# Performance work log

Measured on AMD Instinct MI355X. Metric: run time of the kernel, lower is better.

## Reference

```python
import jax, jax.numpy as jnp
import numpy as np
from jax import lax

H = 64            # hidden size
NUM_LAYERS = 3
EMBED_LEN = 128
B, T = 256, 2048


def _lstm_layer(x, Wih, Whh, bih, bhh):
    """x: [B, T, in]; returns full hidden sequence [B, T, H].
    PyTorch gate order: i, f, g, o."""
    Bn = x.shape[0]
    b = bih + bhh  # [4H]
    # Precompute input contribution for all timesteps: [T, B, 4H]
    xg = jnp.einsum('bti,gi->tbg', x, Wih) + b
    h0 = jnp.zeros((Bn, H), x.dtype)
    c0 = jnp.zeros((Bn, H), x.dtype)

    def step(carry, xg_t):
        h, c = carry
        gates = xg_t + h @ Whh.T  # [B, 4H]
        i, f, g, o = jnp.split(gates, 4, axis=-1)
        i = jax.nn.sigmoid(i)
        f = jax.nn.sigmoid(f)
        g = jnp.tanh(g)
        o = jax.nn.sigmoid(o)
        c = f * c + i * g
        h = o * jnp.tanh(c)
        return (h, c), h

    (_, _), hs = lax.scan(step, (h0, c0), xg)  # hs: [T, B, H]
    return jnp.swapaxes(hs, 0, 1)              # [B, T, H]


def setup_inputs() -> dict:
    key = jax.random.key(0)
    ks = jax.random.split(key, 20)
    k = 1.0 / np.sqrt(H)  # PyTorch default init bound

    def u(kk, shape):
        return jax.random.uniform(kk, shape, jnp.float32, -k, k)

    inp = {"x": jax.random.normal(ks[0], (B, 1, T), jnp.float32)}
    in_sizes = [1, H, H]
    idx = 1
    for l in range(NUM_LAYERS):
        inp[f"Wih{l}"] = u(ks[idx], (4 * H, in_sizes[l])); idx += 1
        inp[f"Whh{l}"] = u(ks[idx], (4 * H, H)); idx += 1
        inp[f"bih{l}"] = u(ks[idx], (4 * H,)); idx += 1
        inp[f"bhh{l}"] = u(ks[idx], (4 * H,)); idx += 1
    inp["fcW"] = u(ks[idx], (EMBED_LEN, H)); idx += 1
    inp["fcb"] = u(ks[idx], (EMBED_LEN,))
    return inp


def reference(x, Wih0, Whh0, bih0, bhh0,
              Wih1, Whh1, bih1, bhh1,
              Wih2, Whh2, bih2, bhh2,
              fcW, fcb):
    # forward: transpose [B,1,T] -> [B,T,1]
    h = jnp.swapaxes(x, 1, 2)
    h = _lstm_layer(h, Wih0, Whh0, bih0, bhh0)
    h = _lstm_layer(h, Wih1, Whh1, bih1, bhh1)
    h = _lstm_layer(h, Wih2, Whh2, bih2, bhh2)
    last = h[:, -1, :]              # [B, H]
    return last @ fcW.T + fcb       # [B, EMBED_LEN]
```

## Files before the change

### kernel.cpp

```cpp
#include <hip/hip_runtime.h>

#define T_LEN 2048
#define HID 64
#define EMB 128
#define WD 8
#define NWIN (T_LEN / WD)
#define NPH (NWIN + 4)

typedef _Float16 half2_t __attribute__((ext_vector_type(2)));
typedef unsigned uint4v __attribute__((ext_vector_type(4)));

#if __has_builtin(__builtin_amdgcn_exp2f)
#define EXP2F(x) __builtin_amdgcn_exp2f(x)
#else
#define EXP2F(x) exp2f(x)
#endif
#if __has_builtin(__builtin_amdgcn_rcpf)
#define RCPF(x) __builtin_amdgcn_rcpf(x)
#else
#define RCPF(x) (1.0f / (x))
#endif

#define LOG2E 1.4426950408889634f

__device__ __forceinline__ float fdot2(unsigned a, unsigned b, float c) {
    return __builtin_amdgcn_fdot2(__builtin_bit_cast(half2_t, a),
                                  __builtin_bit_cast(half2_t, b), c, false);
}

__device__ __forceinline__ float dotrow(const uint4v* w, const uint4v* g, float init) {
    float a0 = init, a1 = 0.f, a2 = 0.f, a3 = 0.f;
    #pragma unroll
    for (int q = 0; q < 8; ++q) {
        a0 = fdot2(w[q][0], g[q][0], a0);
        a1 = fdot2(w[q][1], g[q][1], a1);
        a2 = fdot2(w[q][2], g[q][2], a2);
        a3 = fdot2(w[q][3], g[q][3], a3);
    }
    return (a0 + a1) + (a2 + a3);
}

__device__ __forceinline__ float dot64_i8s(const uint4v* wq, const int* hs,
                                           float fs, float ext) {
    int a0 = 0, a1 = 0, a2 = 0, a3 = 0;
    #pragma unroll
    for (int q = 0; q < 4; ++q) {
        a0 = __builtin_amdgcn_sdot4((int)wq[q][0], hs[4 * q + 0], a0, false);
        a1 = __builtin_amdgcn_sdot4((int)wq[q][1], hs[4 * q + 1], a1, false);
        a2 = __builtin_amdgcn_sdot4((int)wq[q][2], hs[4 * q + 2], a2, false);
        a3 = __builtin_amdgcn_sdot4((int)wq[q][3], hs[4 * q + 3], a3, false);
    }
    int s = (a0 + a1) + (a2 + a3);
    return fmaf((float)s, fs, ext);
}

__device__ __forceinline__ void pack_h(float hf, int lane, int* hs) {
    int qv = (((int)rintf(hf * 127.f)) & 0xff) << (8 * (lane & 3));
    qv |= __builtin_amdgcn_update_dpp(0, qv, 0xB1, 0xf, 0xf, false);
    qv |= __builtin_amdgcn_update_dpp(0, qv, 0x4E, 0xf, 0xf, false);
    #pragma unroll
    for (int k = 0; k < 16; ++k) hs[k] = __builtin_amdgcn_readlane(qv, 4 * k);
}

__device__ __forceinline__ unsigned pack4i8(float4 v, float s) {
    int q0 = (int)rintf(v.x * s), q1 = (int)rintf(v.y * s);
    int q2 = (int)rintf(v.z * s), q3 = (int)rintf(v.w * s);
    return (unsigned)((q0 & 0xff) | ((q1 & 0xff) << 8) |
                      ((q2 & 0xff) << 16) | ((q3 & 0xff) << 24));
}

__device__ __forceinline__ float quant_row(const float* __restrict__ Wp, uint4v* dst) {
    const float4* p = reinterpret_cast<const float4*>(Wp);
    float m = 1e-8f;
    #pragma unroll
    for (int k = 0; k < 16; ++k) {
        float4 v = p[k];
        m = fmaxf(m, fmaxf(fmaxf(fabsf(v.x), fabsf(v.y)),
                           fmaxf(fabsf(v.z), fabsf(v.w))));
    }
    const float s = 127.f / m;
    #pragma unroll
    for (int k = 0; k < 4; ++k) {
        uint4v q;
        q[0] = pack4i8(p[4 * k + 0], s);
        q[1] = pack4i8(p[4 * k + 1], s);
        q[2] = pack4i8(p[4 * k + 2], s);
        q[3] = pack4i8(p[4 * k + 3], s);
        dst[k] = q;
    }
    return m;
}

__device__ __forceinline__ uint4v pack8(float4 a, float4 b, float s) {
    half2_t h0{(_Float16)(a.x * s), (_Float16)(a.y * s)};
    half2_t h1{(_Float16)(a.z * s), (_Float16)(a.w * s)};
    half2_t h2{(_Float16)(b.x * s), (_Float16)(b.y * s)};
    half2_t h3{(_Float16)(b.z * s), (_Float16)(b.w * s)};
    uint4v q;
    q[0] = __builtin_bit_cast(unsigned, h0);
    q[1] = __builtin_bit_cast(unsigned, h1);
    q[2] = __builtin_bit_cast(unsigned, h2);
    q[3] = __builtin_bit_cast(unsigned, h3);
    return q;
}

__device__ __forceinline__ void cvt8(const float* __restrict__ Wp, float s, uint4v* dst) {
    const float4* p = reinterpret_cast<const float4*>(Wp);
    #pragma unroll
    for (int k = 0; k < 8; ++k) dst[k] = pack8(p[2 * k], p[2 * k + 1], s);
}

__global__ __launch_bounds__(512)
__attribute__((amdgpu_waves_per_eu(2, 2)))
void lstm3_fused(
    const float* __restrict__ x,
    const float* __restrict__ Wih0, const float* __restrict__ Whh0,
    const float* __restrict__ bih0, const float* __restrict__ bhh0,
    const float* __restrict__ Wih1, const float* __restrict__ Whh1,
    const float* __restrict__ bih1, const float* __restrict__ bhh1,
    const float* __restrict__ Wih2, const float* __restrict__ Whh2,
    const float* __restrict__ bih2, const float* __restrict__ bhh2,
    const float* __restrict__ fcW,  const float* __restrict__ fcb,
    float* __restrict__ out)
{
    const int b   = blockIdx.x;
    const int tid = threadIdx.x;
    const int wv  = tid >> 6;
    const int L   = tid & 63;

    __shared__ __align__(16) _Float16 h0ring[16][HID];
    __shared__ __align__(16) _Float16 h1ring[16][HID];
    __shared__ __align__(16) _Float16 h2ring[2][HID];
    __shared__ float p1buf[2][WD][4][HID];
    __shared__ float p2buf[2][WD][4][HID];
    __shared__ __align__(16) float xs[T_LEN];

    {
        const float4* xg4 = reinterpret_cast<const float4*>(x + b * T_LEN);
        reinterpret_cast<float4*>(xs)[tid] = xg4[tid];
        reinterpret_cast<unsigned*>(h0ring)[tid] = 0u;
        reinterpret_cast<unsigned*>(h1ring)[tid] = 0u;
        if (tid < 64) reinterpret_cast<unsigned*>(h2ring)[tid] = 0u;
    }

    const float sI = -LOG2E, sF = -LOG2E, sG = -2.f * LOG2E, sO = -LOG2E;
    const float scl[4] = {sI, sF, sG, sO};

    uint4v w[4][8];
    uint4v wq[4][4];
    float bias4[4] = {0.f, 0.f, 0.f, 0.f};
    float wx4[4]   = {0.f, 0.f, 0.f, 0.f};
    float fs4[4]   = {0.f, 0.f, 0.f, 0.f};

    if (wv < 3) {
        const float* Wh = (wv == 0) ? Whh0 : (wv == 1) ? Whh1 : Whh2;
        const float* bi = (wv == 0) ? bih0 : (wv == 1) ? bih1 : bih2;
        const float* bh = (wv == 0) ? bhh0 : (wv == 1) ? bhh1 : bhh2;
        #pragma unroll
        for (int c = 0; c < 4; ++c) {
            float m = quant_row(Wh + (c * 64 + L) * 64, wq[c]);
            fs4[c] = scl[c] * m * (1.f / (127.f * 127.f));
            bias4[c] = (bi[c * 64 + L] + bh[c * 64 + L]) * scl[c];
        }
        if (wv == 0) {
            #pragma unroll
            for (int c = 0; c < 4; ++c) wx4[c] = Wih0[c * 64 + L] * scl[c];
        }
    } else if (wv == 4) {
        cvt8(Wih1 + (  0 + L) * 64, sI, w[0]);
    } else if (wv == 5) {
        cvt8(Wih1 + ( 64 + L) * 64, sF, w[0]);
    } else if (wv == 6) {
        cvt8(Wih1 + (128 + L) * 64, sG, w[0]);
    } else if (wv == 3) {
        cvt8(Wih1 + (192 + L) * 64, sO, w[0]);
        cvt8(Wih2 + (  0 + L) * 64, sI, w[1]);
    } else {
        cvt8(Wih2 + ( 64 + L) * 64, sF, w[0]);
        cvt8(Wih2 + (128 + L) * 64, sG, w[1]);
        cvt8(Wih2 + (192 + L) * 64, sO, w[2]);
    }

    float cst = 0.f;
    int hs[16];
    #pragma unroll
    for (int k = 0; k < 16; ++k) hs[k] = 0;

    __syncthreads();

    for (int ph = 0; ph < NPH; ++ph) {
        const int par = ph & 1;

        if (wv == 0) {
            if (ph < NWIN) {
                const int tb = ph * WD;
                #pragma unroll
                for (int j = 0; j < WD; ++j) {
                    const int r = par * 8 + j;
                    float xv = xs[tb + j];
                    float d0 = dot64_i8s(wq[0], hs, fs4[0], fmaf(wx4[0], xv, bias4[0]));
                    float d1 = dot64_i8s(wq[1], hs, fs4[1], fmaf(wx4[1], xv, bias4[1]));
                    float d2 = dot64_i8s(wq[2], hs, fs4[2], fmaf(wx4[2], xv, bias4[2]));
                    float d3 = dot64_i8s(wq[3], hs, fs4[3], fmaf(wx4[3], xv, bias4[3]));
                    float ai = RCPF(1.f + EXP2F(d0));
                    float af = RCPF(1.f + EXP2F(d1));
                    float ag = fmaf(2.f, RCPF(1.f + EXP2F(d2)), -1.f);
                    float ao = RCPF(1.f + EXP2F(d3));
                    cst = fmaf(af, cst, ai * ag);
                    float tc = fmaf(2.f, RCPF(1.f + EXP2F(-2.f * LOG2E * cst)), -1.f);
                    float hf = ao * tc;
                    h0ring[r][L] = (_Float16)hf;
                    pack_h(hf, L, hs);
                }
            }
        } else if (wv == 1) {
            if (ph >= 2 && ph < NWIN + 2) {
                const float (*pb)[4][HID] = p1buf[par];
                #pragma unroll
                for (int j = 0; j < WD; ++j) {
                    const int r = par * 8 + j;
                    float d0 = dot64_i8s(wq[0], hs, fs4[0], bias4[0] + pb[j][0][L]);
                    float d1 = dot64_i8s(wq[1], hs, fs4[1], bias4[1] + pb[j][1][L]);
                    float d2 = dot64_i8s(wq[2], hs, fs4[2], bias4[2] + pb[j][2][L]);
                    float d3 = dot64_i8s(wq[3], hs, fs4[3], bias4[3] + pb[j][3][L]);
                    float ai = RCPF(1.f + EXP2F(d0));
                    float af = RCPF(1.f + EXP2F(d1));
                    float ag = fmaf(2.f, RCPF(1.f + EXP2F(d2)), -1.f);
                    float ao = RCPF(1.f + EXP2F(d3));
                    cst = fmaf(af, cst, ai * ag);
                    float tc = fmaf(2.f, RCPF(1.f + EXP2F(-2.f * LOG2E * cst)), -1.f);
                    float hf = ao * tc;
                    h1ring[r][L] = (_Float16)hf;
                    pack_h(hf, L, hs);
                }
            }
        } else if (wv == 2) {
            if (ph >= 4) {
                const float (*pb)[4][HID] = p2buf[par];
                #pragma unroll
                for (int j = 0; j < WD; ++j) {
                    float d0 = dot64_i8s(wq[0], hs, fs4[0], bias4[0] + pb[j][0][L]);
                    float d1 = dot64_i8s(wq[1], hs, fs4[1], bias4[1] + pb[j][1][L]);
                    float d2 = dot64_i8s(wq[2], hs, fs4[2], bias4[2] + pb[j][2][L]);
                    float d3 = dot64_i8s(wq[3], hs, fs4[3], bias4[3] + pb[j][3][L]);
                    float ai = RCPF(1.f + EXP2F(d0));
                    float af = RCPF(1.f + EXP2F(d1));
                    float ag = fmaf(2.f, RCPF(1.f + EXP2F(d2)), -1.f);
                    float ao = RCPF(1.f + EXP2F(d3));
                    cst = fmaf(af, cst, ai * ag);
                    float tc = fmaf(2.f, RCPF(1.f + EXP2F(-2.f * LOG2E * cst)), -1.f);
                    float hf = ao * tc;
                    h2ring[j & 1][L] = (_Float16)hf;
                    pack_h(hf, L, hs);
                }
            }
        } else {
            const bool p1act = (ph >= 1 && ph < NWIN + 1);
            const bool p2act = (ph >= 3 && ph < NWIN + 3);
            if (wv == 4 || wv == 5 || wv == 6) {
                if (p1act) {
                    const _Float16* hw = &h0ring[(par ^ 1) * 8][0];
                    float (*po)[4][HID] = p1buf[par ^ 1];
                    const int c0 = wv - 4;
                    #pragma unroll
                    for (int j = 0; j < WD; ++j) {
                        const uint4v* hp = reinterpret_cast<const uint4v*>(hw + j * HID);
                        uint4v g[8];
                        #pragma unroll
                        for (int k = 0; k < 8; ++k) g[k] = hp[k];
                        po[j][c0][L] = dotrow(w[0], g, 0.f);
                    }
                }
            } else if (wv == 3) {
                if (p1act) {
                    const _Float16* hw = &h0ring[(par ^ 1) * 8][0];
                    float (*po)[4][HID] = p1buf[par ^ 1];
                    #pragma unroll
                    for (int j = 0; j < WD; ++j) {
                        const uint4v* hp = reinterpret_cast<const uint4v*>(hw + j * HID);
                        uint4v g[8];
                        #pragma unroll
                        for (int k = 0; k < 8; ++k) g[k] = hp[k];
                        po[j][3][L] = dotrow(w[0], g, 0.f);
                    }
                }
                if (p2act) {
                    const _Float16* hw = &h1ring[(par ^ 1) * 8][0];
                    float (*po)[4][HID] = p2buf[par ^ 1];
                    #pragma unroll
                    for (int j = 0; j < WD; ++j) {
                        const uint4v* hp = reinterpret_cast<const uint4v*>(hw + j * HID);
                        uint4v g[8];
                        #pragma unroll
                        for (int k = 0; k < 8; ++k) g[k] = hp[k];
                        po[j][0][L] = dotrow(w[1], g, 0.f);
                    }
                }
            } else {
                if (p2act) {
                    const _Float16* hw = &h1ring[(par ^ 1) * 8][0];
                    float (*po)[4][HID] = p2buf[par ^ 1];
                    #pragma unroll
                    for (int j = 0; j < WD; ++j) {
                        const uint4v* hp = reinterpret_cast<const uint4v*>(hw + j * HID);
                        uint4v g[8];
                        #pragma unroll
                        for (int k = 0; k < 8; ++k) g[k] = hp[k];
                        po[j][1][L] = dotrow(w[0], g, 0.f);
                        po[j][2][L] = dotrow(w[1], g, 0.f);
                        po[j][3][L] = dotrow(w[2], g, 0.f);
                    }
                }
            }
        }

        __syncthreads();
    }

    if (tid < EMB) {
        float acc = fcb[tid];
        const _Float16* hf = &h2ring[1][0];
        const float4* W4 = reinterpret_cast<const float4*>(fcW + tid * HID);
        #pragma unroll
        for (int k = 0; k < 16; ++k) {
            float4 wv4 = W4[k];
            acc = fmaf(wv4.x, (float)hf[4 * k + 0], acc);
            acc = fmaf(wv4.y, (float)hf[4 * k + 1], acc);
            acc = fmaf(wv4.z, (float)hf[4 * k + 2], acc);
            acc = fmaf(wv4.w, (float)hf[4 * k + 3], acc);
        }
        out[b * EMB + tid] = acc;
    }
}

extern "C" void kernel_launch(void* const* d_in, const int* in_sizes, int n_in,
                              void* d_out, int out_size, void* d_ws, size_t ws_size,
                              hipStream_t stream) {
    const float* x    = (const float*)d_in[0];
    const float* Wih0 = (const float*)d_in[1];
    const float* Whh0 = (const float*)d_in[2];
    const float* bih0 = (const float*)d_in[3];
    const float* bhh0 = (const float*)d_in[4];
    const float* Wih1 = (const float*)d_in[5];
    const float* Whh1 = (const float*)d_in[6];
    const float* bih1 = (const float*)d_in[7];
    const float* bhh1 = (const float*)d_in[8];
    const float* Wih2 = (const float*)d_in[9];
    const float* Whh2 = (const float*)d_in[10];
    const float* bih2 = (const float*)d_in[11];
    const float* bhh2 = (const float*)d_in[12];
    const float* fcW  = (const float*)d_in[13];
    const float* fcb  = (const float*)d_in[14];
    float* out = (float*)d_out;

    lstm3_fused<<<dim3(256), dim3(512), 0, stream>>>(
        x, Wih0, Whh0, bih0, bhh0,
        Wih1, Whh1, bih1, bhh1,
        Wih2, Whh2, bih2, bhh2,
        fcW, fcb, out);
}
```

Measured before the change: 948.4 us.

## Quantize input-projection weights and hidden rings to int8, consolidate onto two waves

The input projections for layers 1 and 2 switch from fp16 dot2 products on five helper waves to int8 sdot4 products. Each projection is now handled by a single wave (wave 3 for layer 1, wave 7 for layer 2), and waves 4-6 go idle. The hidden-state rings in shared memory now store int8 values instead of fp16, which halves shared reads and lets the recurrent waves reuse their existing quantized value. The trade-off is precision: the input-side weights and hidden states lose accuracy from int8 quantization. Also, each remaining helper wave does four rows per step, so it may become the critical path of each phase.

Result: faster. 878.6 us (-7.4%).

```diff
diff --git a/kernel.cpp b/kernel.cpp
--- a/kernel.cpp
+++ b/kernel.cpp
@@ -23,23 +23,6 @@
 
 #define LOG2E 1.4426950408889634f
 
-__device__ __forceinline__ float fdot2(unsigned a, unsigned b, float c) {
-    return __builtin_amdgcn_fdot2(__builtin_bit_cast(half2_t, a),
-                                  __builtin_bit_cast(half2_t, b), c, false);
-}
-
-__device__ __forceinline__ float dotrow(const uint4v* w, const uint4v* g, float init) {
-    float a0 = init, a1 = 0.f, a2 = 0.f, a3 = 0.f;
-    #pragma unroll
-    for (int q = 0; q < 8; ++q) {
-        a0 = fdot2(w[q][0], g[q][0], a0);
-        a1 = fdot2(w[q][1], g[q][1], a1);
-        a2 = fdot2(w[q][2], g[q][2], a2);
-        a3 = fdot2(w[q][3], g[q][3], a3);
-    }
-    return (a0 + a1) + (a2 + a3);
-}
-
 __device__ __forceinline__ float dot64_i8s(const uint4v* wq, const int* hs,
                                            float fs, float ext) {
     int a0 = 0, a1 = 0, a2 = 0, a3 = 0;
@@ -54,8 +37,22 @@
     return fmaf((float)s, fs, ext);
 }
 
-__device__ __forceinline__ void pack_h(float hf, int lane, int* hs) {
-    int qv = (((int)rintf(hf * 127.f)) & 0xff) << (8 * (lane & 3));
+__device__ __forceinline__ float dot64_i8v(const uint4v* wq, const uint4v* g,
+                                           float fs) {
+    int a0 = 0, a1 = 0, a2 = 0, a3 = 0;
+    #pragma unroll
+    for (int q = 0; q < 4; ++q) {
+        a0 = __builtin_amdgcn_sdot4((int)wq[q][0], (int)g[q][0], a0, false);
+        a1 = __builtin_amdgcn_sdot4((int)wq[q][1], (int)g[q][1], a1, false);
+        a2 = __builtin_amdgcn_sdot4((int)wq[q][2], (int)g[q][2], a2, false);
+        a3 = __builtin_amdgcn_sdot4((int)wq[q][3], (int)g[q][3], a3, false);
+    }
+    int s = (a0 + a1) + (a2 + a3);
+    return (float)s * fs;
+}
+
+__device__ __forceinline__ void pack_hq(int qb, int lane, int* hs) {
+    int qv = (qb & 0xff) << (8 * (lane & 3));
     qv |= __builtin_amdgcn_update_dpp(0, qv, 0xB1, 0xf, 0xf, false);
     qv |= __builtin_amdgcn_update_dpp(0, qv, 0x4E, 0xf, 0xf, false);
     #pragma unroll
@@ -89,25 +86,6 @@
         dst[k] = q;
     }
     return m;
-}
-
-__device__ __forceinline__ uint4v pack8(float4 a, float4 b, float s) {
-    half2_t h0{(_Float16)(a.x * s), (_Float16)(a.y * s)};
-    half2_t h1{(_Float16)(a.z * s), (_Float16)(a.w * s)};
-    half2_t h2{(_Float16)(b.x * s), (_Float16)(b.y * s)};
-    half2_t h3{(_Float16)(b.z * s), (_Float16)(b.w * s)};
-    uint4v q;
-    q[0] = __builtin_bit_cast(unsigned, h0);
-    q[1] = __builtin_bit_cast(unsigned, h1);
-    q[2] = __builtin_bit_cast(unsigned, h2);
-    q[3] = __builtin_bit_cast(unsigned, h3);
-    return q;
-}
-
-__device__ __forceinline__ void cvt8(const float* __restrict__ Wp, float s, uint4v* dst) {
-    const float4* p = reinterpret_cast<const float4*>(Wp);
-    #pragma unroll
-    for (int k = 0; k < 8; ++k) dst[k] = pack8(p[2 * k], p[2 * k + 1], s);
 }
 
 __global__ __launch_bounds__(512)
@@ -128,8 +106,8 @@
     const int wv  = tid >> 6;
     const int L   = tid & 63;
 
-    __shared__ __align__(16) _Float16 h0ring[16][HID];
-    __shared__ __align__(16) _Float16 h1ring[16][HID];
+    __shared__ __align__(16) signed char h0q[16][HID];
+    __shared__ __align__(16) signed char h1q[16][HID];
     __shared__ __align__(16) _Float16 h2ring[2][HID];
     __shared__ float p1buf[2][WD][4][HID];
     __shared__ float p2buf[2][WD][4][HID];
@@ -138,15 +116,16 @@
     {
         const float4* xg4 = reinterpret_cast<const float4*>(x + b * T_LEN);
         reinterpret_cast<float4*>(xs)[tid] = xg4[tid];
-        reinterpret_cast<unsigned*>(h0ring)[tid] = 0u;
-        reinterpret_cast<unsigned*>(h1ring)[tid] = 0u;
+        if (tid < 256) {
+            reinterpret_cast<unsigned*>(h0q)[tid] = 0u;
+            reinterpret_cast<unsigned*>(h1q)[tid] = 0u;
+        }
         if (tid < 64) reinterpret_cast<unsigned*>(h2ring)[tid] = 0u;
     }
 
     const float sI = -LOG2E, sF = -LOG2E, sG = -2.f * LOG2E, sO = -LOG2E;
     const float scl[4] = {sI, sF, sG, sO};
 
-    uint4v w[4][8];
     uint4v wq[4][4];
     float bias4[4] = {0.f, 0.f, 0.f, 0.f};
     float wx4[4]   = {0.f, 0.f, 0.f, 0.f};
@@ -166,19 +145,13 @@
             #pragma unroll
             for (int c = 0; c < 4; ++c) wx4[c] = Wih0[c * 64 + L] * scl[c];
         }
-    } else if (wv == 4) {
-        cvt8(Wih1 + (  0 + L) * 64, sI, w[0]);
-    } else if (wv == 5) {
-        cvt8(Wih1 + ( 64 + L) * 64, sF, w[0]);
-    } else if (wv == 6) {
-        cvt8(Wih1 + (128 + L) * 64, sG, w[0]);
-    } else if (wv == 3) {
-        cvt8(Wih1 + (192 + L) * 64, sO, w[0]);
-        cvt8(Wih2 + (  0 + L) * 64, sI, w[1]);
-    } else {
-        cvt8(Wih2 + ( 64 + L) * 64, sF, w[0]);
-        cvt8(Wih2 + (128 + L) * 64, sG, w[1]);
-        cvt8(Wih2 + (192 + L) * 64, sO, w[2]);
+    } else if (wv == 3 || wv == 7) {
+        const float* Wsrc = (wv == 3) ? Wih1 : Wih2;
+        #pragma unroll
+        for (int c = 0; c < 4; ++c) {
+            float m = quant_row(Wsrc + (c * 64 + L) * 64, wq[c]);
+            fs4[c] = scl[c] * m * (1.f / (127.f * 127.f));
+        }
     }
 
     float cst = 0.f;
@@ -209,8 +182,9 @@
                     cst = fmaf(af, cst, ai * ag);
                     float tc = fmaf(2.f, RCPF(1.f + EXP2F(-2.f * LOG2E * cst)), -1.f);
                     float hf = ao * tc;
-                    h0ring[r][L] = (_Float16)hf;
-                    pack_h(hf, L, hs);
+                    int qb = (int)rintf(hf * 127.f);
+                    h0q[r][L] = (signed char)qb;
+                    pack_hq(qb, L, hs);
                 }
             }
         } else if (wv == 1) {
@@ -230,8 +204,9 @@
                     cst = fmaf(af, cst, ai * ag);
                     float tc = fmaf(2.f, RCPF(1.f + EXP2F(-2.f * LOG2E * cst)), -1.f);
                     float hf = ao * tc;
-                    h1ring[r][L] = (_Float16)hf;
-                    pack_h(hf, L, hs);
+                    int qb = (int)rintf(hf * 127.f);
+                    h1q[r][L] = (signed char)qb;
+                    pack_hq(qb, L, hs);
                 }
             }
         } else if (wv == 2) {
@@ -251,65 +226,36 @@
                     float tc = fmaf(2.f, RCPF(1.f + EXP2F(-2.f * LOG2E * cst)), -1.f);
                     float hf = ao * tc;
                     h2ring[j & 1][L] = (_Float16)hf;
-                    pack_h(hf, L, hs);
-                }
-            }
-        } else {
-            const bool p1act = (ph >= 1 && ph < NWIN + 1);
-            const bool p2act = (ph >= 3 && ph < NWIN + 3);
-            if (wv == 4 || wv == 5 || wv == 6) {
-                if (p1act) {
-                    const _Float16* hw = &h0ring[(par ^ 1) * 8][0];
-                    float (*po)[4][HID] = p1buf[par ^ 1];
-                    const int c0 = wv - 4;
-                    #pragma unroll
-                    for (int j = 0; j < WD; ++j) {
-                        const uint4v* hp = reinterpret_cast<const uint4v*>(hw + j * HID);
-                        uint4v g[8];
-                        #pragma unroll
-                        for (int k = 0; k < 8; ++k) g[k] = hp[k];
-                        po[j][c0][L] = dotrow(w[0], g, 0.f);
-                    }
-                }
-            } else if (wv == 3) {
-                if (p1act) {
-                    const _Float16* hw = &h0ring[(par ^ 1) * 8][0];
-                    float (*po)[4][HID] = p1buf[par ^ 1];
-                    #pragma unroll
-                    for (int j = 0; j < WD; ++j) {
-                        const uint4v* hp = reinterpret_cast<const uint4v*>(hw + j * HID);
-                        uint4v g[8];
-                        #pragma unroll
-                        for (int k = 0; k < 8; ++k) g[k] = hp[k];
-                        po[j][3][L] = dotrow(w[0], g, 0.f);
-                    }
-                }
-                if (p2act) {
-                    const _Float16* hw = &h1ring[(par ^ 1) * 8][0];
-                    float (*po)[4][HID] = p2buf[par ^ 1];
-                    #pragma unroll
-                    for (int j = 0; j < WD; ++j) {
-                        const uint4v* hp = reinterpret_cast<const uint4v*>(hw + j * HID);
-                        uint4v g[8];
-                        #pragma unroll
-                        for (int k = 0; k < 8; ++k) g[k] = hp[k];
-                        po[j][0][L] = dotrow(w[1], g, 0.f);
-                    }
-                }
-            } else {
-                if (p2act) {
-                    const _Float16* hw = &h1ring[(par ^ 1) * 8][0];
-                    float (*po)[4][HID] = p2buf[par ^ 1];
-                    #pragma unroll
-                    for (int j = 0; j < WD; ++j) {
-                        const uint4v* hp = reinterpret_cast<const uint4v*>(hw + j * HID);
-                        uint4v g[8];
-                        #pragma unroll
-                        for (int k = 0; k < 8; ++k) g[k] = hp[k];
-                        po[j][1][L] = dotrow(w[0], g, 0.f);
-                        po[j][2][L] = dotrow(w[1], g, 0.f);
-                        po[j][3][L] = dotrow(w[2], g, 0.f);
-                    }
+                    int qb = (int)rintf(hf * 127.f);
+                    pack_hq(qb, L, hs);
+                }
+            }
+        } else if (wv == 3) {
+            if (ph >= 1 && ph < NWIN + 1) {
+                float (*po)[4][HID] = p1buf[par ^ 1];
+                const signed char* hw = &h0q[(par ^ 1) * 8][0];
+                #pragma unroll
+                for (int j = 0; j < WD; ++j) {
+                    const uint4v* g = reinterpret_cast<const uint4v*>(hw + j * HID);
+                    uint4v gq[4] = {g[0], g[1], g[2], g[3]};
+                    po[j][0][L] = dot64_i8v(wq[0], gq, fs4[0]);
+                    po[j][1][L] = dot64_i8v(wq[1], gq, fs4[1]);
+                    po[j][2][L] = dot64_i8v(wq[2], gq, fs4[2]);
+                    po[j][3][L] = dot64_i8v(wq[3], gq, fs4[3]);
+                }
+            }
+        } else if (wv == 7) {
+            if (ph >= 3 && ph < NWIN + 3) {
+                float (*po)[4][HID] = p2buf[par ^ 1];
+                const signed char* hw = &h1q[(par ^ 1) * 8][0];
+                #pragma unroll
+                for (int j = 0; j < WD; ++j) {
+                    const uint4v* g = reinterpret_cast<const uint4v*>(hw + j * HID);
+                    uint4v gq[4] = {g[0], g[1], g[2], g[3]};
+                    po[j][0][L] = dot64_i8v(wq[0], gq, fs4[0]);
+                    po[j][1][L] = dot64_i8v(wq[1], gq, fs4[1]);
+                    po[j][2][L] = dot64_i8v(wq[2], gq, fs4[2]);
+                    po[j][3][L] = dot64_i8v(wq[3], gq, fs4[3]);
                 }
             }
         }
```
